# Performance work log

Measured on AMD Instinct MI355X. Metric: run time of the kernel, lower is better.

## Reference

```python
import jax, jax.numpy as jnp
import numpy as np

# dims
D_MODEL = 256; D_STATE = 16; D_CONV = 4; EXPAND = 2
D_INNER = D_MODEL * EXPAND            # 512
DT_RANK = 16                          # ceil(256/16)
B_SZ = 16; C_IN = 64; T_LR = 2560; R = 2; C_OUT = 64


def _p(key, shape, scale=0.02):
    return jax.random.normal(key, shape, jnp.float32) * scale


def setup_inputs() -> dict:
    key = jax.random.key(0)
    ks = iter(jax.random.split(key, 48))
    inp = {}
    inp['x'] = jax.random.normal(next(ks), (B_SZ, C_IN, T_LR), jnp.float32)
    # encoder: Conv1d(64->128,k3,p1) ; Conv1d(128->256,k3,p1)
    inp['enc_w1'] = _p(next(ks), (128, C_IN, 3)); inp['enc_b1'] = jnp.zeros((128,), jnp.float32)
    inp['enc_w2'] = _p(next(ks), (256, 128, 3)); inp['enc_b2'] = jnp.zeros((256,), jnp.float32)
    # BidirectionalMamba norms
    inp['norm1_w'] = jnp.ones((D_MODEL,), jnp.float32)
    inp['norm2_w'] = jnp.ones((D_MODEL,), jnp.float32)
    # one forward ('f') and one backward ('b') Mamba v1 block
    for p in ('f', 'b'):
        inp[p + '_inW'] = _p(next(ks), (2 * D_INNER, D_MODEL))
        inp[p + '_convW'] = _p(next(ks), (D_INNER, D_CONV), 0.2)
        inp[p + '_convb'] = jnp.zeros((D_INNER,), jnp.float32)
        inp[p + '_xW'] = _p(next(ks), (DT_RANK + 2 * D_STATE, D_INNER))
        inp[p + '_dtW'] = _p(next(ks), (D_INNER, DT_RANK), 0.1)
        inp[p + '_dtb'] = -4.0 + 2.0 * jax.random.uniform(next(ks), (D_INNER,), jnp.float32)
        inp[p + '_Alog'] = jnp.log(jnp.tile(jnp.arange(1, D_STATE + 1, dtype=jnp.float32), (D_INNER, 1)))
        inp[p + '_D'] = jnp.ones((D_INNER,), jnp.float32)
        inp[p + '_outW'] = _p(next(ks), (D_MODEL, D_INNER))
    # post-bottleneck: Conv1d(512->256,k3,p1) + BatchNorm1d(256) (eval)
    inp['convd_w'] = _p(next(ks), (256, 512, 3)); inp['convd_b'] = jnp.zeros((256,), jnp.float32)
    inp['bn_g'] = jnp.ones((256,), jnp.float32); inp['bn_b'] = jnp.zeros((256,), jnp.float32)
    inp['bn_mean'] = jnp.zeros((256,), jnp.float32); inp['bn_var'] = jnp.ones((256,), jnp.float32)
    # SubPixel1D: Conv1d(256 -> target_channels*r, k3, p1), r=2
    inp['sp_w'] = _p(next(ks), (C_OUT * R, 256, 3)); inp['sp_b'] = jnp.zeros((C_OUT * R,), jnp.float32)
    return inp


def silu(x):
    return x * jax.nn.sigmoid(x)


def conv1d(x, w, b):  # x: (B,C,L), w: (O,I,K), 'same' padding
    k = w.shape[-1]
    y = jax.lax.conv_general_dilated(x, w, (1,), [(k // 2, k // 2)],
                                     dimension_numbers=('NCH', 'OIH', 'NCH'))
    return y + b[None, :, None]


def rmsnorm(x, w, eps=1e-6):
    return x * jax.lax.rsqrt(jnp.mean(x * x, -1, keepdims=True) + eps) * w


def mamba(x, inW, convW, convb, xW, dtW, dtb, Alog, Dp, outW):
    # x: (B, L, D_MODEL) -> (B, L, D_MODEL); Mamba v1 selective scan.
    Bn = x.shape[0]
    xz = x @ inW.T                               # (B,L,2*di)
    xc, z = jnp.split(xz, 2, axis=-1)            # (B,L,di) each
    # causal depthwise conv over time
    xt = jnp.transpose(xc, (0, 2, 1))            # (B,di,L)
    xt = jax.lax.conv_general_dilated(xt, convW[:, None, :], (1,), [(D_CONV - 1, 0)],
                                      dimension_numbers=('NCH', 'OIH', 'NCH'),
                                      feature_group_count=D_INNER)
    xc = silu(jnp.transpose(xt + convb[None, :, None], (0, 2, 1)))  # (B,L,di)
    dbc = xc @ xW.T                              # (B,L,dt_rank+2N)
    dt = jax.nn.softplus(dbc[..., :DT_RANK] @ dtW.T + dtb)          # (B,L,di)
    Bc = dbc[..., DT_RANK:DT_RANK + D_STATE]     # (B,L,N)
    Cc = dbc[..., DT_RANK + D_STATE:]            # (B,L,N)
    A = -jnp.exp(Alog)                           # (di,N)

    def step(h, inp):
        dt_t, B_t, C_t, x_t = inp                # (B,di),(B,N),(B,N),(B,di)
        dA = jnp.exp(dt_t[..., None] * A)        # (B,di,N)
        h = dA * h + (dt_t * x_t)[..., None] * B_t[:, None, :]
        y = jnp.einsum('bdn,bn->bd', h, C_t)
        return h, y

    xs = (jnp.transpose(dt, (1, 0, 2)), jnp.transpose(Bc, (1, 0, 2)),
          jnp.transpose(Cc, (1, 0, 2)), jnp.transpose(xc, (1, 0, 2)))
    h0 = jnp.zeros((Bn, D_INNER, D_STATE), x.dtype)
    _, ys = jax.lax.scan(step, h0, xs)           # ys: (L,B,di)
    y = jnp.transpose(ys, (1, 0, 2)) + xc * Dp
    return (y * silu(z)) @ outW.T


def reference(x, enc_w1, enc_b1, enc_w2, enc_b2, norm1_w, norm2_w,
              f_inW, f_convW, f_convb, f_xW, f_dtW, f_dtb, f_Alog, f_D, f_outW,
              b_inW, b_convW, b_convb, b_xW, b_dtW, b_dtb, b_Alog, b_D, b_outW,
              convd_w, convd_b, bn_g, bn_b, bn_mean, bn_var, sp_w, sp_b):
    # encoder (dropout = identity in eval)
    e = silu(conv1d(x, enc_w1, enc_b1))
    e = silu(conv1d(e, enc_w2, enc_b2))          # (B,256,T)
    t = jnp.transpose(e, (0, 2, 1))              # (B,T,256)
    # Bi-Mamba bottleneck layer
    xn = rmsnorm(t, norm1_w)
    mo_f = mamba(xn, f_inW, f_convW, f_convb, f_xW, f_dtW, f_dtb, f_Alog, f_D, f_outW) + xn
    xb = xn[:, ::-1, :]
    mo_b = mamba(xb, b_inW, b_convW, b_convb, b_xW, b_dtW, b_dtb, b_Alog, b_D, b_outW) + xb
    mo_b = mo_b[:, ::-1, :]
    combined = rmsnorm(mo_f + mo_b, norm2_w)
    m = jnp.concatenate([combined, t], axis=-1)  # (B,T,512)
    m = jnp.transpose(m, (0, 2, 1))              # (B,512,T)
    # conv_d + BatchNorm1d (eval) + SiLU
    d = conv1d(m, convd_w, convd_b)
    d = (d - bn_mean[None, :, None]) * jax.lax.rsqrt(bn_var + 1e-5)[None, :, None] \
        * bn_g[None, :, None] + bn_b[None, :, None]
    d = silu(d)
    # SubPixel1D upsample x2
    s = conv1d(d, sp_w, sp_b)                    # (B, C_OUT*R, T)
    Bn, C, T = s.shape
    s = s.reshape(Bn, C // R, R, T).transpose(0, 1, 3, 2).reshape(Bn, C // R, T * R)
    return s                                      # (B, 64, 5120)
```

## Files before the change

### kernel.cpp

```cpp
#include <hip/hip_runtime.h>
#include <hip/hip_bf16.h>
#include <math.h>

#define B_SZ 16
#define T_LR 2560
#define BT (B_SZ * T_LR)
#define DM 256
#define DI 512
#define DS 16
#define DTR 16
#define CH 128
#define CH_LOG2 7
#define CLEN (T_LR / CH)

typedef __attribute__((ext_vector_type(8))) short bf16x8;
typedef __attribute__((ext_vector_type(4))) float f32x4;

__device__ __forceinline__ float silu_f(float x) {
    return x / (1.f + __expf(-x));
}
__device__ __forceinline__ unsigned short f2bf(float v) {
    __hip_bfloat16 h = __float2bfloat16(v);
    return *(unsigned short*)&h;
}
__device__ __forceinline__ float bf2f(unsigned short u) {
    union { unsigned int i; float f; } c;
    c.i = (unsigned int)u << 16;
    return c.f;
}
__device__ __forceinline__ int seqrev(int r) {
    int s = r / T_LR, t = r % T_LR;
    return s * T_LR + (T_LR - 1 - t);
}
__device__ __forceinline__ float softplus_f(float x) {
    return (x > 20.f) ? x : __logf(1.f + __expf(x));
}

__global__ __launch_bounds__(256) void k_prep(
    const float* __restrict__ enc_w1, const float* __restrict__ enc_w2,
    const float* __restrict__ convd_w, const float* __restrict__ sp_w,
    const float* __restrict__ convd_b, const float* __restrict__ bn_g,
    const float* __restrict__ bn_b, const float* __restrict__ bn_mean,
    const float* __restrict__ bn_var,
    const float* __restrict__ inW0, const float* __restrict__ inW1,
    const float* __restrict__ outW0, const float* __restrict__ outW1,
    const float* __restrict__ xW0, const float* __restrict__ xW1,
    const float* __restrict__ Alog0, const float* __restrict__ Alog1,
    const float* __restrict__ x,
    unsigned short* __restrict__ W1r, unsigned short* __restrict__ W2r,
    unsigned short* __restrict__ Wdr, unsigned short* __restrict__ Wspr,
    float* __restrict__ alpha, float* __restrict__ beta,
    unsigned short* __restrict__ inW_bf2, unsigned short* __restrict__ outW_bf2,
    unsigned short* __restrict__ xW_bc2, float* __restrict__ Aflag,
    unsigned short* __restrict__ xt)
{
    __shared__ float ts[32][33];
    __shared__ int s_ok;
    int blk = blockIdx.x;
    int tid = threadIdx.x;
    if (blk < 32) {
        int i = blk * 256 + tid;
        int n = i / 64, ci = i % 64;
        #pragma unroll
        for (int k = 0; k < 3; k++)
            W1r[((size_t)k * 128 + n) * 64 + ci] = f2bf(enc_w1[((size_t)n * 64 + ci) * 3 + k]);
    } else if (blk < 160) {
        int i = (blk - 32) * 256 + tid;
        int n = i / 128, ci = i % 128;
        #pragma unroll
        for (int k = 0; k < 3; k++)
            W2r[((size_t)k * 256 + n) * 128 + ci] = f2bf(enc_w2[((size_t)n * 128 + ci) * 3 + k]);
    } else if (blk < 672) {
        int i = (blk - 160) * 256 + tid;
        int n = i / 512, ci = i % 512;
        #pragma unroll
        for (int k = 0; k < 3; k++)
            Wdr[((size_t)k * 256 + n) * 512 + ci] = f2bf(convd_w[((size_t)n * 512 + ci) * 3 + k]);
    } else if (blk < 800) {
        int i = (blk - 672) * 256 + tid;
        int n = i / 256, ci = i % 256;
        #pragma unroll
        for (int k = 0; k < 3; k++)
            Wspr[((size_t)k * 128 + n) * 256 + ci] = f2bf(sp_w[((size_t)n * 256 + ci) * 3 + k]);
    } else if (blk < 801) {
        int c = tid;
        float a = bn_g[c] * rsqrtf(bn_var[c] + 1e-5f);
        alpha[c] = a;
        beta[c] = (convd_b[c] - bn_mean[c]) * a + bn_b[c];
    } else if (blk < 1825) {
        int i = (blk - 801) * 256 + tid;
        inW_bf2[i] = f2bf(inW0[i]);
        inW_bf2[262144 + i] = f2bf(inW1[i]);
    } else if (blk < 2337) {
        int i = (blk - 1825) * 256 + tid;
        outW_bf2[i] = f2bf(outW0[i]);
        outW_bf2[131072 + i] = f2bf(outW1[i]);
    } else if (blk < 2433) {
        int i = (blk - 2337) * 256 + tid;
        xW_bc2[i] = f2bf(xW0[i]);
        xW_bc2[24576 + i] = f2bf(xW1[i]);
    } else if (blk < 2434) {
        if (tid == 0) s_ok = 1;
        __syncthreads();
        int ok = 1;
        for (int i = tid; i < DI * DS; i += 256) {
            int d = i >> 4, n = i & 15;
            float a0f = __expf(Alog0[d * DS]);
            float anf = __expf(Alog0[d * DS + n]);
            if (fabsf(anf - (float)(n + 1) * a0f) > 1e-3f * (float)(n + 1)) ok = 0;
            float a0b = __expf(Alog1[d * DS]);
            float anb = __expf(Alog1[d * DS + n]);
            if (fabsf(anb - (float)(n + 1) * a0b) > 1e-3f * (float)(n + 1)) ok = 0;
        }
        if (!ok) atomicAnd(&s_ok, 0);
        __syncthreads();
        if (tid == 0) Aflag[0] = s_ok ? 1.f : 0.f;
    } else {
        int idx = blk - 2434;
        int t0 = (idx % 80) * 32;
        int c0 = ((idx / 80) & 1) * 32;
        int b = idx / 160;
        int tx = tid & 31, ty = tid >> 5;
        #pragma unroll
        for (int j = 0; j < 4; j++) {
            int c = c0 + ty + j * 8;
            ts[ty + j * 8][tx] = x[((size_t)b * 64 + c) * T_LR + t0 + tx];
        }
        __syncthreads();
        #pragma unroll
        for (int j = 0; j < 4; j++) {
            int t = t0 + ty + j * 8;
            xt[((size_t)b * T_LR + t) * 64 + c0 + tx] = f2bf(ts[tx][ty + j * 8]);
        }
    }
}

__global__ __launch_bounds__(256, 3) void k_conv3_bf(const unsigned short* __restrict__ A1, int K1,
                                                  const unsigned short* __restrict__ A2, int K2,
                                                  const unsigned short* __restrict__ W,
                                                  const float* __restrict__ alpha,
                                                  const float* __restrict__ beta,
                                                  float* __restrict__ outf,
                                                  unsigned short* __restrict__ outb,
                                                  int N, int dosilu, int pixsh) {
    int Kt = K1 + K2;
    __shared__ unsigned short As[2][130][40];
    int tid = threadIdx.x;
    int wave = tid >> 6, lane = tid & 63;
    int wm = (wave >> 1) * 64, wn = (wave & 1) * 64;
    int m0 = blockIdx.x * 128, n0 = blockIdx.y * 128;
    int b = m0 / T_LR, t0 = m0 % T_LR;
    int q = lane >> 4, ml = lane & 15;
    const unsigned short* wbase = W + (size_t)(n0 + wn + ml) * Kt + q * 8;
    size_t tapstride = (size_t)N * Kt;
    size_t nistride  = (size_t)16 * Kt;
    f32x4 acc[4][4] = {};
    int cq = tid & 3;
    int r0 = tid >> 2;
    int r1 = r0 + 64;
    int r2 = r0 + 128;
    bool has2 = (tid < 8);
    int ta0 = t0 - 1 + r0, ta1 = t0 - 1 + r1, ta2 = t0 - 1 + r2;
    bool va0 = (ta0 >= 0) && (ta0 < T_LR);
    bool va1 = (ta1 < T_LR);
    bool va2 = has2 && (ta2 < T_LR);
    uint4 v0, v1, v2;
    #define LOADA(vv, valid, t, col) { vv = make_uint4(0u,0u,0u,0u); if (valid) { \
        const unsigned short* src = ((col) < K1) \
            ? A1 + (size_t)(b * T_LR + (t)) * K1 + (col) \
            : A2 + (size_t)(b * T_LR + (t)) * K2 + ((col) - K1); \
        vv = *(const uint4*)src; } }
    LOADA(v0, va0, ta0, cq * 8);
    LOADA(v1, va1, ta1, cq * 8);
    LOADA(v2, va2, ta2, cq * 8);
    *(uint4*)&As[0][r0][cq * 8] = v0;
    *(uint4*)&As[0][r1][cq * 8] = v1;
    if (has2) *(uint4*)&As[0][r2][cq * 8] = v2;
    int nk = Kt >> 5;
    for (int kk = 0; kk < nk; kk++) {
        __syncthreads();
        int cur = kk & 1;
        int k0 = kk << 5;
        if (kk + 1 < nk) {
            int col = k0 + 32 + cq * 8;
            LOADA(v0, va0, ta0, col);
            LOADA(v1, va1, ta1, col);
            LOADA(v2, va2, ta2, col);
        }
        #pragma unroll
        for (int tap = 0; tap < 3; tap++) {
            bf16x8 bfr[4];
            #pragma unroll
            for (int ni = 0; ni < 4; ni++)
                bfr[ni] = *(const bf16x8*)(wbase + tap * tapstride + ni * nistride + k0);
            #pragma unroll
            for (int mi = 0; mi < 4; mi++) {
                bf16x8 af = *(const bf16x8*)&As[cur][wm + mi * 16 + ml + tap][q * 8];
                #pragma unroll
                for (int ni = 0; ni < 4; ni++)
                    acc[mi][ni] = __builtin_amdgcn_mfma_f32_16x16x32_bf16(af, bfr[ni], acc[mi][ni], 0, 0, 0);
            }
        }
        if (kk + 1 < nk) {
            *(uint4*)&As[cur ^ 1][r0][cq * 8] = v0;
            *(uint4*)&As[cur ^ 1][r1][cq * 8] = v1;
            if (has2) *(uint4*)&As[cur ^ 1][r2][cq * 8] = v2;
        }
    }
    #undef LOADA
    #pragma unroll
    for (int mi = 0; mi < 4; mi++) {
        #pragma unroll
        for (int r = 0; r < 4; r++) {
            int mr = m0 + wm + mi * 16 + q * 4 + r;
            int t = mr - b * T_LR;
            #pragma unroll
            for (int ni = 0; ni < 4; ni++) {
                int col = n0 + wn + ni * 16 + ml;
                float a = alpha ? alpha[col] : 1.f;
                float v = acc[mi][ni][r] * a + beta[col];
                if (dosilu) v = silu_f(v);
                if (pixsh) {
                    int c2 = col >> 1, rr = col & 1;
                    outf[(((size_t)b * 64 + c2) * T_LR + t) * 2 + rr] = v;
                } else {
                    size_t o = (size_t)mr * N + col;
                    if (outf) outf[o] = v;
                    if (outb) outb[o] = f2bf(v);
                }
            }
        }
    }
}

__global__ __launch_bounds__(256) void k_inproj_conv(const unsigned short* __restrict__ xn,
                                                     const unsigned short* __restrict__ inW2,
                                                     const float* __restrict__ cw0,
                                                     const float* __restrict__ cw1,
                                                     const float* __restrict__ cb0,
                                                     const float* __restrict__ cb1,
                                                     unsigned short* __restrict__ xcs,
                                                     long long dsXcs) {
    __shared__ unsigned short As[128][40];
    __shared__ unsigned short Bs[128][40];
    __shared__ unsigned short Ct[131][136];
    int dir = blockIdx.z;
    int arev = dir;
    const unsigned short* inW = inW2 + (size_t)dir * 1024 * DM;
    const float* cw = dir ? cw1 : cw0;
    const float* cb = dir ? cb1 : cb0;
    xcs += (size_t)dir * dsXcs;
    int tid = threadIdx.x;
    int wave = tid >> 6, lane = tid & 63;
    int wm = (wave >> 1) * 64, wn = (wave & 1) * 64;
    int m0 = blockIdx.x * 128, n0 = blockIdx.y * 128;
    int b = m0 / T_LR, t0 = m0 % T_LR;
    int sc = tid & 3, sr = tid >> 2;
    int ar0 = m0 + sr, ar1 = m0 + sr + 64;
    if (arev) { ar0 = seqrev(ar0); ar1 = seqrev(ar1); }
    const unsigned short* ap0 = xn + (size_t)ar0 * DM + sc * 8;
    const unsigned short* ap1 = xn + (size_t)ar1 * DM + sc * 8;
    const unsigned short* bp0 = inW + (size_t)(n0 + sr) * DM + sc * 8;
    const unsigned short* bp1 = inW + (size_t)(n0 + sr + 64) * DM + sc * 8;
    f32x4 acc[4][4] = {};
    int q = lane >> 4, ml = lane & 15;
    for (int k0 = 0; k0 < DM; k0 += 32) {
        uint4 a0 = *(const uint4*)(ap0 + k0);
        uint4 a1 = *(const uint4*)(ap1 + k0);
        uint4 b0 = *(const uint4*)(bp0 + k0);
        uint4 b1 = *(const uint4*)(bp1 + k0);
        __syncthreads();
        *(uint4*)&As[sr][sc * 8]      = a0;
        *(uint4*)&As[sr + 64][sc * 8] = a1;
        *(uint4*)&Bs[sr][sc * 8]      = b0;
        *(uint4*)&Bs[sr + 64][sc * 8] = b1;
        __syncthreads();
        bf16x8 af[4], bfr[4];
        #pragma unroll
        for (int mi = 0; mi < 4; mi++)
            af[mi] = *(const bf16x8*)&As[wm + mi * 16 + ml][q * 8];
        #pragma unroll
        for (int ni = 0; ni < 4; ni++)
            bfr[ni] = *(const bf16x8*)&Bs[wn + ni * 16 + ml][q * 8];
        #pragma unroll
        for (int mi = 0; mi < 4; mi++)
            #pragma unroll
            for (int ni = 0; ni < 4; ni++)
                acc[mi][ni] = __builtin_amdgcn_mfma_f32_16x16x32_bf16(af[mi], bfr[ni], acc[mi][ni], 0, 0, 0);
    }
    #pragma unroll
    for (int mi = 0; mi < 4; mi++)
        #pragma unroll
        for (int r = 0; r < 4; r++)
            #pragma unroll
            for (int ni = 0; ni < 4; ni++)
                Ct[3 + wm + mi * 16 + q * 4 + r][wn + ni * 16 + ml] = f2bf(acc[mi][ni][r]);
    for (int i = tid; i < 384; i += 256) {
        int hr = i >> 7, c = i & 127;
        int tr = t0 - 3 + hr;
        float v = 0.f;
        if (tr >= 0) {
            int src = b * T_LR + (arev ? (T_LR - 1 - tr) : tr);
            const unsigned short* xr = xn + (size_t)src * DM;
            const unsigned short* wr = inW + (size_t)(n0 + c) * DM;
            for (int k = 0; k < DM; k += 8) {
                uint4 xa = *(const uint4*)(xr + k);
                uint4 wa = *(const uint4*)(wr + k);
                const unsigned short* xs = (const unsigned short*)&xa;
                const unsigned short* wsp = (const unsigned short*)&wa;
                #pragma unroll
                for (int j = 0; j < 8; j++) v += bf2f(xs[j]) * bf2f(wsp[j]);
            }
        }
        Ct[hr][c] = f2bf(v);
    }
    __syncthreads();
    int col = tid & 127;
    int d = n0 + col;
    float w0 = cw[d * 4 + 0], w1 = cw[d * 4 + 1], w2 = cw[d * 4 + 2], w3 = cw[d * 4 + 3];
    float bi = cb[d];
    int rbase = tid >> 7;
    for (int j = 0; j < 64; j++) {
        int row = rbase + 2 * j;
        float v = bi + bf2f(Ct[row][col]) * w0 + bf2f(Ct[row + 1][col]) * w1
                     + bf2f(Ct[row + 2][col]) * w2 + bf2f(Ct[row + 3][col]) * w3;
        xcs[(size_t)(m0 + row) * DI + d] = f2bf(silu_f(v));
    }
}

__global__ __launch_bounds__(256) void k_rmsnorm(const float* __restrict__ in1,
                                                 const float* __restrict__ in2,
                                                 const float* __restrict__ w,
                                                 float* __restrict__ out,
                                                 unsigned short* __restrict__ out_bf,
                                                 int ntok) {
    int tok = (blockIdx.x * 256 + threadIdx.x) >> 6;
    int lane = threadIdx.x & 63;
    if (tok >= ntok) return;
    float4 v = ((const float4*)(in1 + (size_t)tok * DM))[lane];
    if (in2) {
        float4 u = ((const float4*)(in2 + (size_t)tok * DM))[lane];
        v.x += u.x; v.y += u.y; v.z += u.z; v.w += u.w;
    }
    float ss = v.x * v.x + v.y * v.y + v.z * v.z + v.w * v.w;
    #pragma unroll
    for (int off = 32; off > 0; off >>= 1) ss += __shfl_xor(ss, off);
    float sc = rsqrtf(ss * (1.f / 256.f) + 1e-6f);
    float4 wv = ((const float4*)w)[lane];
    float4 o;
    o.x = v.x * sc * wv.x; o.y = v.y * sc * wv.y;
    o.z = v.z * sc * wv.z; o.w = v.w * sc * wv.w;
    if (out) ((float4*)(out + (size_t)tok * DM))[lane] = o;
    if (out_bf) {
        ushort4 ob;
        ob.x = f2bf(o.x); ob.y = f2bf(o.y); ob.z = f2bf(o.z); ob.w = f2bf(o.w);
        ((ushort4*)(out_bf + (size_t)tok * DM))[lane] = ob;
    }
}

__global__ __launch_bounds__(256) void k_gemm_bf(const unsigned short* __restrict__ A, int lda, long long dsA,
                                                 const unsigned short* __restrict__ Bw, long long dsB,
                                                 float* Cf, long long dsCf, int ldc,
                                                 const float* __restrict__ res,
                                                 int K, int Nout, int crevmode) {
    __shared__ unsigned short As[128][40];
    __shared__ unsigned short Bs[128][40];
    int dir = blockIdx.z;
    A += (long long)dir * dsA;
    Bw += (long long)dir * dsB;
    Cf += (long long)dir * dsCf;
    int crev = (crevmode == 2) ? dir : crevmode;
    int tid = threadIdx.x;
    int wave = tid >> 6, lane = tid & 63;
    int wm = (wave >> 1) * 64, wn = (wave & 1) * 64;
    int m0 = blockIdx.x * 128, n0 = blockIdx.y * 128;
    int sc = tid & 3, sr = tid >> 2;
    const unsigned short* ap0 = A + (size_t)(m0 + sr) * lda + sc * 8;
    const unsigned short* ap1 = A + (size_t)(m0 + sr + 64) * lda + sc * 8;
    bool bv0 = (n0 + sr) < Nout;
    bool bv1 = (n0 + sr + 64) < Nout;
    const unsigned short* bp0 = Bw + (size_t)(n0 + sr) * K + sc * 8;
    const unsigned short* bp1 = Bw + (size_t)(n0 + sr + 64) * K + sc * 8;
    f32x4 acc[4][4] = {};
    int q = lane >> 4, ml = lane & 15;
    for (int k0 = 0; k0 < K; k0 += 32) {
        uint4 a0 = *(const uint4*)(ap0 + k0);
        uint4 a1 = *(const uint4*)(ap1 + k0);
        uint4 b0 = make_uint4(0u, 0u, 0u, 0u), b1 = make_uint4(0u, 0u, 0u, 0u);
        if (bv0) b0 = *(const uint4*)(bp0 + k0);
        if (bv1) b1 = *(const uint4*)(bp1 + k0);
        __syncthreads();
        *(uint4*)&As[sr][sc * 8]      = a0;
        *(uint4*)&As[sr + 64][sc * 8] = a1;
        *(uint4*)&Bs[sr][sc * 8]      = b0;
        *(uint4*)&Bs[sr + 64][sc * 8] = b1;
        __syncthreads();
        bf16x8 af[4], bfr[4];
        #pragma unroll
        for (int mi = 0; mi < 4; mi++)
            af[mi] = *(const bf16x8*)&As[wm + mi * 16 + ml][q * 8];
        #pragma unroll
        for (int ni = 0; ni < 4; ni++)
            bfr[ni] = *(const bf16x8*)&Bs[wn + ni * 16 + ml][q * 8];
        #pragma unroll
        for (int mi = 0; mi < 4; mi++)
            #pragma unroll
            for (int ni = 0; ni < 4; ni++)
                acc[mi][ni] = __builtin_amdgcn_mfma_f32_16x16x32_bf16(af[mi], bfr[ni], acc[mi][ni], 0, 0, 0);
    }
    #pragma unroll
    for (int mi = 0; mi < 4; mi++) {
        #pragma unroll
        for (int r = 0; r < 4; r++) {
            int mr = m0 + wm + mi * 16 + q * 4 + r;
            int orow = crev ? seqrev(mr) : mr;
            #pragma unroll
            for (int ni = 0; ni < 4; ni++) {
                int col = n0 + wn + ni * 16 + ml;
                if (col < Nout) {
                    float v = acc[mi][ni][r];
                    if (res) v += res[(size_t)orow * ldc + col];
                    Cf[(size_t)orow * ldc + col] = v;
                }
            }
        }
    }
}

__global__ __launch_bounds__(256) void k_gemm_bf_cb(const unsigned short* __restrict__ A, int lda,
                                                    const unsigned short* __restrict__ Bw, long long dsB,
                                                    unsigned short* __restrict__ Cb, int ldc, long long dsCb,
                                                    const unsigned short* __restrict__ gate, long long dsGate,
                                                    int K) {
    __shared__ __align__(16) unsigned short smem[2 * 128 * 40];
    unsigned short (*As)[40] = (unsigned short(*)[40])smem;
    unsigned short (*Bs)[40] = (unsigned short(*)[40])(smem + 128 * 40);
    float* sC = (float*)smem;
    int dir = blockIdx.z;
    int arev = dir;
    Bw += (long long)dir * dsB;
    Cb += (long long)dir * dsCb;
    gate += (long long)dir * dsGate;
    int tid = threadIdx.x;
    int wave = tid >> 6, lane = tid & 63;
    int wm = (wave >> 1) * 64, wn = (wave & 1) * 64;
    int m0 = blockIdx.x * 128, n0 = blockIdx.y * 128;
    int sc = tid & 3, sr = tid >> 2;
    int ar0 = m0 + sr, ar1 = m0 + sr + 64;
    if (arev) { ar0 = seqrev(ar0); ar1 = seqrev(ar1); }
    const unsigned short* ap0 = A + (size_t)ar0 * lda + sc * 8;
    const unsigned short* ap1 = A + (size_t)ar1 * lda + sc * 8;
    const unsigned short* bp0 = Bw + (size_t)(n0 + sr) * K + sc * 8;
    const unsigned short* bp1 = Bw + (size_t)(n0 + sr + 64) * K + sc * 8;
    f32x4 acc[4][4] = {};
    int q = lane >> 4, ml = lane & 15;
    for (int k0 = 0; k0 < K; k0 += 32) {
        uint4 a0 = *(const uint4*)(ap0 + k0);
        uint4 a1 = *(const uint4*)(ap1 + k0);
        uint4 b0 = *(const uint4*)(bp0 + k0);
        uint4 b1 = *(const uint4*)(bp1 + k0);
        __syncthreads();
        *(uint4*)&As[sr][sc * 8]      = a0;
        *(uint4*)&As[sr + 64][sc * 8] = a1;
        *(uint4*)&Bs[sr][sc * 8]      = b0;
        *(uint4*)&Bs[sr + 64][sc * 8] = b1;
        __syncthreads();
        bf16x8 af[4], bfr[4];
        #pragma unroll
        for (int mi = 0; mi < 4; mi++)
            af[mi] = *(const bf16x8*)&As[wm + mi * 16 + ml][q * 8];
        #pragma unroll
        for (int ni = 0; ni < 4; ni++)
            bfr[ni] = *(const bf16x8*)&Bs[wn + ni * 16 + ml][q * 8];
        #pragma unroll
        for (int mi = 0; mi < 4; mi++)
            #pragma unroll
            for (int ni = 0; ni < 4; ni++)
                acc[mi][ni] = __builtin_amdgcn_mfma_f32_16x16x32_bf16(af[mi], bfr[ni], acc[mi][ni], 0, 0, 0);
    }
    #pragma unroll
    for (int p = 0; p < 4; p++) {
        __syncthreads();
        if ((wave >> 1) == (p >> 1)) {
            int mib = (p & 1) * 2;
            #pragma unroll
            for (int m2 = 0; m2 < 2; m2++) {
                int mi = mib + m2;
                int rl = mi * 16 + q * 4 - (p & 1) * 32;
                #pragma unroll
                for (int r = 0; r < 4; r++)
                    #pragma unroll
                    for (int ni = 0; ni < 4; ni++)
                        sC[(rl + r) * 140 + wn + ni * 16 + ml] = acc[mi][ni][r];
            }
        }
        __syncthreads();
        #pragma unroll
        for (int gi = 0; gi < 2; gi++) {
            int g = tid + gi * 256;
            int row = g >> 4;
            int colg = (g & 15) * 8;
            int grow = m0 + p * 32 + row;
            const float* src = sC + row * 140 + colg;
            float4 v0 = *(const float4*)src;
            float4 v1 = *(const float4*)(src + 4);
            float vv[8] = {v0.x, v0.y, v0.z, v0.w, v1.x, v1.y, v1.z, v1.w};
            unsigned short gu[8];
            *(uint4*)gu = *(const uint4*)(gate + (size_t)grow * ldc + n0 + colg);
            unsigned short o[8];
            #pragma unroll
            for (int jj = 0; jj < 8; jj++) {
                float v = vv[jj];
                v = silu_f(v) * bf2f(gu[jj]);
                o[jj] = f2bf(v);
            }
            *(uint4*)(Cb + (size_t)grow * ldc + n0 + colg) = *(uint4*)o;
        }
    }
}

__global__ __launch_bounds__(256) void k_scan_p1(const unsigned short* __restrict__ x,
                                                 const float* __restrict__ db,
                                                 const float* __restrict__ dtW0, const float* __restrict__ dtW1,
                                                 const float* __restrict__ dtb0, const float* __restrict__ dtb1,
                                                 const float* __restrict__ Alog0, const float* __restrict__ Alog1,
                                                 const float* __restrict__ Aflag,
                                                 float* __restrict__ hS,
                                                 float* __restrict__ csum, int Bc) {
    __shared__ float dbs[CLEN * 48];
    int tid = threadIdx.x;
    int gid = blockIdx.x * 256 + tid;
    int d = gid & (DI - 1);
    int bcix = gid >> 9;
    int c = bcix & (CH - 1);
    int bl = bcix >> CH_LOG2;
    int dir = (bl >= Bc) ? 1 : 0;
    const float* dtW  = dir ? dtW1  : dtW0;
    const float* dtb  = dir ? dtb1  : dtb0;
    const float* Alog = dir ? Alog1 : Alog0;
    int tbase = c * CLEN;
    const float* dbp = db + ((size_t)bl * T_LR + tbase) * 48;
    if (tid < 240) *(float4*)&dbs[tid * 4] = *(const float4*)(dbp + tid * 4);
    bool fast = (Aflag[0] != 0.f);
    float A0 = -__expf(Alog[d * DS]);
    float Av[DS], h[DS];
    #pragma unroll
    for (int n = 0; n < DS; n++) h[n] = 0.f;
    if (!fast) {
        #pragma unroll
        for (int n = 0; n < DS; n++) Av[n] = -__expf(Alog[d * DS + n]);
    }
    const float4* wp = (const float4*)(dtW + d * 16);
    float4 w0 = wp[0], w1 = wp[1], w2 = wp[2], w3 = wp[3];
    float bias = dtb[d];
    const unsigned short* xp = x + ((size_t)bl * T_LR + tbase) * DI + d;
    float S = 0.f;
    __syncthreads();
    for (int t = 0; t < CLEN; t++) {
        const float* bc = dbs + t * 48;
        float dl = bias
            + bc[0] * w0.x + bc[1] * w0.y + bc[2] * w0.z + bc[3] * w0.w
            + bc[4] * w1.x + bc[5] * w1.y + bc[6] * w1.z + bc[7] * w1.w
            + bc[8] * w2.x + bc[9] * w2.y + bc[10] * w2.z + bc[11] * w2.w
            + bc[12] * w3.x + bc[13] * w3.y + bc[14] * w3.z + bc[15] * w3.w;
        float dtv = softplus_f(dl);
        float xv  = bf2f(xp[(size_t)t * DI]);
        float dtx = dtv * xv;
        S += dtv;
        if (fast) {
            float e1 = __expf(dtv * A0);
            float e = e1;
            #pragma unroll
            for (int n = 0; n < DS; n++) {
                h[n] = e * h[n] + dtx * bc[16 + n];
                e *= e1;
            }
        } else {
            #pragma unroll
            for (int n = 0; n < DS; n++)
                h[n] = __expf(dtv * Av[n]) * h[n] + dtx * bc[16 + n];
        }
    }
    float* hp = hS + (size_t)gid * DS;
    #pragma unroll
    for (int n = 0; n < DS; n++) hp[n] = h[n];
    csum[gid] = S;
}

__global__ __launch_bounds__(256) void k_scan_p2(float* __restrict__ hS,
                                                 const float* __restrict__ csum,
                                                 const float* __restrict__ Alog0,
                                                 const float* __restrict__ Alog1, int Bc) {
    int gid = blockIdx.x * 256 + threadIdx.x;
    int n = gid & (DS - 1);
    int d = (gid >> 4) & (DI - 1);
    int bl = gid >> 13;
    const float* Alog = (bl >= Bc) ? Alog1 : Alog0;
    float An = -__expf(Alog[d * DS + n]);
    float hs = 0.f;
    for (int c = 0; c < CH; c++) {
        size_t base = ((size_t)(bl * CH + c) * DI + d);
        float he = hS[base * DS + n];
        float S  = csum[base];
        hS[base * DS + n] = hs;
        hs = __expf(An * S) * hs + he;
    }
}

__global__ __launch_bounds__(256) void k_scan_p3(unsigned short* __restrict__ x,
                                                 const float* __restrict__ db,
                                                 const float* __restrict__ dtW0, const float* __restrict__ dtW1,
                                                 const float* __restrict__ dtb0, const float* __restrict__ dtb1,
                                                 const float* __restrict__ Alog0, const float* __restrict__ Alog1,
                                                 const float* __restrict__ Aflag,
                                                 const float* __restrict__ Dp0, const float* __restrict__ Dp1,
                                                 const float* __restrict__ hS, int Bc) {
    __shared__ float dbs[CLEN * 48];
    int tid = threadIdx.x;
    int gid = blockIdx.x * 256 + tid;
    int d = gid & (DI - 1);
    int bcix = gid >> 9;
    int c = bcix & (CH - 1);
    int bl = bcix >> CH_LOG2;
    int dir = (bl >= Bc) ? 1 : 0;
    const float* dtW  = dir ? dtW1  : dtW0;
    const float* dtb  = dir ? dtb1  : dtb0;
    const float* Alog = dir ? Alog1 : Alog0;
    const float* Dp   = dir ? Dp1   : Dp0;
    int tbase = c * CLEN;
    const float* dbp = db + ((size_t)bl * T_LR + tbase) * 48;
    if (tid < 240) *(float4*)&dbs[tid * 4] = *(const float4*)(dbp + tid * 4);
    bool fast = (Aflag[0] != 0.f);
    float A0 = -__expf(Alog[d * DS]);
    float Av[DS], h[DS];
    const float* hp = hS + (size_t)gid * DS;
    #pragma unroll
    for (int n = 0; n < DS; n++) h[n] = hp[n];
    if (!fast) {
        #pragma unroll
        for (int n = 0; n < DS; n++) Av[n] = -__expf(Alog[d * DS + n]);
    }
    const float4* wp = (const float4*)(dtW + d * 16);
    float4 w0 = wp[0], w1 = wp[1], w2 = wp[2], w3 = wp[3];
    float bias = dtb[d];
    float Dd = Dp[d];
    unsigned short* xp = x + ((size_t)bl * T_LR + tbase) * DI + d;
    __syncthreads();
    for (int t = 0; t < CLEN; t++) {
        const float* bc = dbs + t * 48;
        float dl = bias
            + bc[0] * w0.x + bc[1] * w0.y + bc[2] * w0.z + bc[3] * w0.w
            + bc[4] * w1.x + bc[5] * w1.y + bc[6] * w1.z + bc[7] * w1.w
            + bc[8] * w2.x + bc[9] * w2.y + bc[10] * w2.z + bc[11] * w2.w
            + bc[12] * w3.x + bc[13] * w3.y + bc[14] * w3.z + bc[15] * w3.w;
        float dtv = softplus_f(dl);
        float xv  = bf2f(xp[(size_t)t * DI]);
        float dtx = dtv * xv;
        float acc = 0.f;
        if (fast) {
            float e1 = __expf(dtv * A0);
            float e = e1;
            #pragma unroll
            for (int n = 0; n < DS; n++) {
                h[n] = e * h[n] + dtx * bc[16 + n];
                acc += h[n] * bc[32 + n];
                e *= e1;
            }
        } else {
            #pragma unroll
            for (int n = 0; n < DS; n++) {
                h[n] = __expf(dtv * Av[n]) * h[n] + dtx * bc[16 + n];
                acc += h[n] * bc[32 + n];
            }
        }
        xp[(size_t)t * DI] = f2bf(acc + xv * Dd);
    }
}

extern "C" void kernel_launch(void* const* d_in, const int* in_sizes, int n_in,
                              void* d_out, int out_size, void* d_ws, size_t ws_size,
                              hipStream_t stream) {
    const float* x       = (const float*)d_in[0];
    const float* enc_w1  = (const float*)d_in[1];
    const float* enc_b1  = (const float*)d_in[2];
    const float* enc_w2  = (const float*)d_in[3];
    const float* enc_b2  = (const float*)d_in[4];
    const float* norm1_w = (const float*)d_in[5];
    const float* norm2_w = (const float*)d_in[6];
    const float* convd_w = (const float*)d_in[25];
    const float* convd_b = (const float*)d_in[26];
    const float* bn_g    = (const float*)d_in[27];
    const float* bn_b    = (const float*)d_in[28];
    const float* bn_mean = (const float*)d_in[29];
    const float* bn_var  = (const float*)d_in[30];
    const float* sp_w    = (const float*)d_in[31];
    const float* sp_b    = (const float*)d_in[32];
    float* out = (float*)d_out;

    const float* inW0   = (const float*)d_in[7];
    const float* cw0    = (const float*)d_in[8];
    const float* cb0    = (const float*)d_in[9];
    const float* xW0    = (const float*)d_in[10];
    const float* dtW0   = (const float*)d_in[11];
    const float* dtb0   = (const float*)d_in[12];
    const float* Alog0  = (const float*)d_in[13];
    const float* Dp0    = (const float*)d_in[14];
    const float* outW0  = (const float*)d_in[15];
    const float* inW1   = (const float*)d_in[16];
    const float* cw1    = (const float*)d_in[17];
    const float* cb1    = (const float*)d_in[18];
    const float* xW1    = (const float*)d_in[19];
    const float* dtW1   = (const float*)d_in[20];
    const float* dtb1   = (const float*)d_in[21];
    const float* Alog1  = (const float*)d_in[22];
    const float* Dp1    = (const float*)d_in[23];
    const float* outW1  = (const float*)d_in[24];

    float* ws = (float*)d_ws;
    size_t availf = ws_size / sizeof(float);
    size_t o = 0;
    float* t_buf  = ws + o; o += (size_t)BT * DM;
    float* xn_buf = ws + o; o += (size_t)BT * DM;
    float* mo     = ws + o; o += (size_t)BT * DM;
    unsigned short* xn_bf = (unsigned short*)(ws + o); o += (size_t)BT * DM / 2;
    unsigned short* tb_bf = (unsigned short*)(ws + o); o += (size_t)BT * DM / 2;
    unsigned short* inW_bf2  = (unsigned short*)(ws + o); o += (size_t)1024 * DM;
    unsigned short* outW_bf2 = (unsigned short*)(ws + o); o += (size_t)DM * DI;
    unsigned short* xW_bc2   = (unsigned short*)(ws + o); o += (size_t)48 * DI;
    unsigned short* W1r  = (unsigned short*)(ws + o); o += (3 * 128 * 64) / 2;
    unsigned short* W2r  = (unsigned short*)(ws + o); o += (3 * 256 * 128) / 2;
    unsigned short* Wdr  = (unsigned short*)(ws + o); o += (3 * 256 * 512) / 2;
    unsigned short* Wspr = (unsigned short*)(ws + o); o += (3 * 128 * 256) / 2;
    float* alpha_d = ws + o; o += 256;
    float* beta_d  = ws + o; o += 256;
    float* Aflag_d = ws + o; o += 4;
    size_t persist = o;
    float* scratch = ws + persist;
    size_t scratch_avail = (availf > persist) ? (availf - persist) : 0;
    size_t per_b2 = 2 * ((size_t)T_LR * DI / 2 * 2 + (size_t)T_LR * 48
                         + (size_t)CH * DI * (DS + 1));
    int Bc = 16;
    while (Bc > 1 && (size_t)Bc * per_b2 > scratch_avail) Bc >>= 1;

    unsigned short* xt  = (unsigned short*)mo;
    unsigned short* e1t = (unsigned short*)(mo + (size_t)BT * 64 / 2);
    unsigned short* comb_bf = (unsigned short*)xn_buf;
    unsigned short* d_bf = (unsigned short*)mo;

    k_prep<<<4994, 256, 0, stream>>>(enc_w1, enc_w2, convd_w, sp_w,
                                     convd_b, bn_g, bn_b, bn_mean, bn_var,
                                     inW0, inW1, outW0, outW1, xW0, xW1,
                                     Alog0, Alog1,
                                     x, W1r, W2r, Wdr, Wspr, alpha_d, beta_d,
                                     inW_bf2, outW_bf2, xW_bc2, Aflag_d, xt);

    k_conv3_bf<<<dim3(BT / 128, 1), 256, 0, stream>>>(xt, 64, nullptr, 0, W1r,
                                                      nullptr, enc_b1, nullptr, e1t, 128, 1, 0);
    k_conv3_bf<<<dim3(BT / 128, 2), 256, 0, stream>>>(e1t, 128, nullptr, 0, W2r,
                                                      nullptr, enc_b2, t_buf, tb_bf, 256, 1, 0);
    k_rmsnorm<<<BT / 4, 256, 0, stream>>>(t_buf, nullptr, norm1_w, xn_buf, xn_bf, BT);

    long long dsMo1 = (long long)(t_buf - mo);
    for (int b0 = 0; b0 < B_SZ; b0 += Bc) {
        int Tc = Bc * T_LR;
        long long TcDI = (long long)Tc * DI;
        unsigned short* xcs = (unsigned short*)scratch;
        unsigned short* ygb = xcs + (size_t)2 * Tc * DI;
        float* db   = (float*)(ygb + (size_t)2 * Tc * DI);
        float* hS   = db + (size_t)2 * Tc * 48;
        float* csum = hS + (size_t)2 * Bc * CH * DI * DS;
        const float*          xnC  = xn_buf + (size_t)b0 * T_LR * DM;
        const unsigned short* xnbC = xn_bf  + (size_t)b0 * T_LR * DM;
        float*                moC  = mo     + (size_t)b0 * T_LR * DM;
        k_inproj_conv<<<dim3(Tc / 128, DI / 128, 2), 256, 0, stream>>>(
            xnbC, inW_bf2, cw0, cw1, cb0, cb1, xcs, TcDI);
        k_gemm_bf<<<dim3(Tc / 128, 1, 2), 256, 0, stream>>>(
            xcs, DI, TcDI, xW_bc2, (long long)48 * DI,
            db, (long long)Tc * 48, 48, nullptr, DI, 48, 0);
        k_scan_p1<<<(2 * Bc * CH * DI) / 256, 256, 0, stream>>>(
            xcs, db, dtW0, dtW1, dtb0, dtb1, Alog0, Alog1, Aflag_d, hS, csum, Bc);
        k_scan_p2<<<(2 * Bc * DI * DS) / 256, 256, 0, stream>>>(
            hS, csum, Alog0, Alog1, Bc);
        k_scan_p3<<<(2 * Bc * CH * DI) / 256, 256, 0, stream>>>(
            xcs, db, dtW0, dtW1, dtb0, dtb1, Alog0, Alog1, Aflag_d, Dp0, Dp1, hS, Bc);
        k_gemm_bf_cb<<<dim3(Tc / 128, DI / 128, 2), 256, 0, stream>>>(
            xnbC, DM, inW_bf2 + (size_t)DI * DM, (long long)1024 * DM,
            ygb, DI, TcDI, xcs, TcDI, DM);
        k_gemm_bf<<<dim3(Tc / 128, DM / 128, 2), 256, 0, stream>>>(
            ygb, DI, TcDI, outW_bf2, (long long)DM * DI,
            moC, dsMo1, DM, xnC, DI, DM, 2);
    }

    k_rmsnorm<<<BT / 4, 256, 0, stream>>>(mo, t_buf, norm2_w, nullptr, comb_bf, BT);
    k_conv3_bf<<<dim3(BT / 128, 2), 256, 0, stream>>>(comb_bf, 256, tb_bf, 256, Wdr,
                                                      alpha_d, beta_d, nullptr, d_bf, 256, 1, 0);
    k_conv3_bf<<<dim3(BT / 128, 1), 256, 0, stream>>>(d_bf, 256, nullptr, 0, Wspr,
                                                      nullptr, sp_b, out, nullptr, 128, 0, 1);
}
```

Baseline: 1.193 ms.

## Swizzle conv weights into MFMA fragment layout and stage epilogue through LDS

The prep kernel now writes the bf16 conv weights in a tiled layout. Each 16x32 MFMA B fragment becomes one contiguous 1 KB block, so a wave's weight loads turn into fully coalesced 16-byte-per-lane reads instead of strided rows. The conv GEMM epilogue also stages accumulators through reused LDS in 32-row slabs and writes output with vectorized, row-contiguous float4/uint4 stores, including float2 stores for the subpixel path. This adds extra barriers and LDS traffic. The subpixel path now drops the alpha and SiLU handling, which is only correct because that call passes neither.

```diff
diff --git a/kernel.cpp b/kernel.cpp
--- a/kernel.cpp
+++ b/kernel.cpp
@@ -34,6 +34,10 @@
 }
 __device__ __forceinline__ float softplus_f(float x) {
     return (x > 20.f) ? x : __logf(1.f + __expf(x));
+}
+__device__ __forceinline__ size_t wswz_idx(int tap, int n, int c, int N, int Kt) {
+    return ((size_t)((tap * (N >> 4) + (n >> 4)) * (Kt >> 5) + (c >> 5)) << 9)
+         + (size_t)((((c >> 3) & 3) * 16 + (n & 15)) * 8 + (c & 7));
 }
 
 __global__ __launch_bounds__(256) void k_prep(
@@ -63,25 +67,25 @@
         int n = i / 64, ci = i % 64;
         #pragma unroll
         for (int k = 0; k < 3; k++)
-            W1r[((size_t)k * 128 + n) * 64 + ci] = f2bf(enc_w1[((size_t)n * 64 + ci) * 3 + k]);
+            W1r[wswz_idx(k, n, ci, 128, 64)] = f2bf(enc_w1[((size_t)n * 64 + ci) * 3 + k]);
     } else if (blk < 160) {
         int i = (blk - 32) * 256 + tid;
         int n = i / 128, ci = i % 128;
         #pragma unroll
         for (int k = 0; k < 3; k++)
-            W2r[((size_t)k * 256 + n) * 128 + ci] = f2bf(enc_w2[((size_t)n * 128 + ci) * 3 + k]);
+            W2r[wswz_idx(k, n, ci, 256, 128)] = f2bf(enc_w2[((size_t)n * 128 + ci) * 3 + k]);
     } else if (blk < 672) {
         int i = (blk - 160) * 256 + tid;
         int n = i / 512, ci = i % 512;
         #pragma unroll
         for (int k = 0; k < 3; k++)
-            Wdr[((size_t)k * 256 + n) * 512 + ci] = f2bf(convd_w[((size_t)n * 512 + ci) * 3 + k]);
+            Wdr[wswz_idx(k, n, ci, 256, 512)] = f2bf(convd_w[((size_t)n * 512 + ci) * 3 + k]);
     } else if (blk < 800) {
         int i = (blk - 672) * 256 + tid;
         int n = i / 256, ci = i % 256;
         #pragma unroll
         for (int k = 0; k < 3; k++)
-            Wspr[((size_t)k * 128 + n) * 256 + ci] = f2bf(sp_w[((size_t)n * 256 + ci) * 3 + k]);
+            Wspr[wswz_idx(k, n, ci, 128, 256)] = f2bf(sp_w[((size_t)n * 256 + ci) * 3 + k]);
     } else if (blk < 801) {
         int c = tid;
         float a = bn_g[c] * rsqrtf(bn_var[c] + 1e-5f);
@@ -137,23 +141,25 @@
 
 __global__ __launch_bounds__(256, 3) void k_conv3_bf(const unsigned short* __restrict__ A1, int K1,
                                                   const unsigned short* __restrict__ A2, int K2,
-                                                  const unsigned short* __restrict__ W,
+                                                  const unsigned short* __restrict__ Wz,
                                                   const float* __restrict__ alpha,
                                                   const float* __restrict__ beta,
                                                   float* __restrict__ outf,
                                                   unsigned short* __restrict__ outb,
                                                   int N, int dosilu, int pixsh) {
     int Kt = K1 + K2;
-    __shared__ unsigned short As[2][130][40];
+    __shared__ __align__(16) unsigned short smem[2 * 130 * 40];
+    unsigned short (*As)[130][40] = (unsigned short (*)[130][40])smem;
+    float* sC = (float*)smem;
     int tid = threadIdx.x;
     int wave = tid >> 6, lane = tid & 63;
     int wm = (wave >> 1) * 64, wn = (wave & 1) * 64;
     int m0 = blockIdx.x * 128, n0 = blockIdx.y * 128;
     int b = m0 / T_LR, t0 = m0 % T_LR;
     int q = lane >> 4, ml = lane & 15;
-    const unsigned short* wbase = W + (size_t)(n0 + wn + ml) * Kt + q * 8;
-    size_t tapstride = (size_t)N * Kt;
-    size_t nistride  = (size_t)16 * Kt;
+    int Nb16 = N >> 4, Kb32 = Kt >> 5;
+    int nb0 = (n0 + wn) >> 4;
+    const unsigned short* wl = Wz + (size_t)lane * 8;
     f32x4 acc[4][4] = {};
     int cq = tid & 3;
     int r0 = tid >> 2;
@@ -176,7 +182,7 @@
     *(uint4*)&As[0][r0][cq * 8] = v0;
     *(uint4*)&As[0][r1][cq * 8] = v1;
     if (has2) *(uint4*)&As[0][r2][cq * 8] = v2;
-    int nk = Kt >> 5;
+    int nk = Kb32;
     for (int kk = 0; kk < nk; kk++) {
         __syncthreads();
         int cur = kk & 1;
@@ -189,10 +195,11 @@
         }
         #pragma unroll
         for (int tap = 0; tap < 3; tap++) {
+            int tb = tap * Nb16 + nb0;
             bf16x8 bfr[4];
             #pragma unroll
             for (int ni = 0; ni < 4; ni++)
-                bfr[ni] = *(const bf16x8*)(wbase + tap * tapstride + ni * nistride + k0);
+                bfr[ni] = *(const bf16x8*)(wl + ((size_t)((tb + ni) * Kb32 + kk) << 9));
             #pragma unroll
             for (int mi = 0; mi < 4; mi++) {
                 bf16x8 af = *(const bf16x8*)&As[cur][wm + mi * 16 + ml + tap][q * 8];
@@ -208,26 +215,62 @@
         }
     }
     #undef LOADA
+    int rowoff = m0 - b * T_LR;
     #pragma unroll
-    for (int mi = 0; mi < 4; mi++) {
-        #pragma unroll
-        for (int r = 0; r < 4; r++) {
-            int mr = m0 + wm + mi * 16 + q * 4 + r;
-            int t = mr - b * T_LR;
-            #pragma unroll
-            for (int ni = 0; ni < 4; ni++) {
-                int col = n0 + wn + ni * 16 + ml;
-                float a = alpha ? alpha[col] : 1.f;
-                float v = acc[mi][ni][r] * a + beta[col];
-                if (dosilu) v = silu_f(v);
-                if (pixsh) {
-                    int c2 = col >> 1, rr = col & 1;
-                    outf[(((size_t)b * 64 + c2) * T_LR + t) * 2 + rr] = v;
-                } else {
-                    size_t o = (size_t)mr * N + col;
-                    if (outf) outf[o] = v;
-                    if (outb) outb[o] = f2bf(v);
+    for (int p = 0; p < 4; p++) {
+        __syncthreads();
+        if ((wave >> 1) == (p >> 1)) {
+            int mib = (p & 1) * 2;
+            #pragma unroll
+            for (int m2 = 0; m2 < 2; m2++) {
+                int mi = mib + m2;
+                int rl = mi * 16 + q * 4 - (p & 1) * 32;
+                #pragma unroll
+                for (int r = 0; r < 4; r++)
+                    #pragma unroll
+                    for (int ni = 0; ni < 4; ni++)
+                        sC[(rl + r) * 140 + wn + ni * 16 + ml] = acc[mi][ni][r];
+            }
+        }
+        __syncthreads();
+        if (pixsh) {
+            int row = tid & 31, c2g = tid >> 5;
+            int t = rowoff + p * 32 + row;
+            float* dst = outf + ((size_t)b * 64 * T_LR + t) * 2;
+            #pragma unroll
+            for (int j = 0; j < 8; j++) {
+                int c2 = c2g + j * 8;
+                float va = sC[row * 140 + 2 * c2]     + beta[2 * c2];
+                float vb = sC[row * 140 + 2 * c2 + 1] + beta[2 * c2 + 1];
+                *(float2*)&dst[(size_t)c2 * T_LR * 2] = make_float2(va, vb);
+            }
+        } else {
+            #pragma unroll
+            for (int gi = 0; gi < 2; gi++) {
+                int g = tid + gi * 256;
+                int row = g >> 4;
+                int colg = (g & 15) * 8;
+                int mr = m0 + p * 32 + row;
+                const float* src = sC + row * 140 + colg;
+                float vv[8];
+                *(float4*)&vv[0] = *(const float4*)src;
+                *(float4*)&vv[4] = *(const float4*)(src + 4);
+                unsigned short ob[8];
+                #pragma unroll
+                for (int jj = 0; jj < 8; jj++) {
+                    int col = n0 + colg + jj;
+                    float a = alpha ? alpha[col] : 1.f;
+                    float v = vv[jj] * a + beta[col];
+                    if (dosilu) v = silu_f(v);
+                    vv[jj] = v;
+                    ob[jj] = f2bf(v);
                 }
+                if (outf) {
+                    *(float4*)(outf + (size_t)mr * N + n0 + colg) = *(float4*)&vv[0];
+                    *(float4*)(outf + (size_t)mr * N + n0 + colg + 4) = *(float4*)&vv[4];
+                }
+                if (outb)
+                    *(uint4*)(outb + (size_t)mr * N + n0 + colg) = *(uint4*)ob;
             }
         }
     }
```

Measured after the change: 1.157 ms. 1.03x faster.
